# Optimization experiments

Hardware: AMD Instinct MI355X
Metric: run time of the kernel (lower is better)

The kernel has to match this reference:

```python
import jax, jax.numpy as jnp
import numpy as np

C = 128   # channels / dim
NH = 4    # num heads
HD = C // NH
K = 5     # conv kernel size: t=int((log2(128)+1)/2)=4 -> k=5
P = 12    # patch size
GH = 8    # grid height/width (96/12)
NPATCH = GH * GH
FEAT = P * P * C


def _ln(x, g, b):
    m = jnp.mean(x, -1, keepdims=True)
    v = jnp.var(x, -1, keepdims=True)
    return (x - m) / jnp.sqrt(v + 1e-5) * g + b


def _conv1d(x, w, pad):
    return jax.lax.conv_general_dilated(x, w, (1,), [(pad, pad)], dimension_numbers=('NCH', 'OIH', 'NCH'))


def _pool(x, out):
    # exact adaptive avg pool when H % out == 0
    B, c, H, W = x.shape
    f = H // out
    return x.reshape(B, c, out, f, out, f).mean((3, 5))


def _bilinear_ac(x, out):
    # bilinear interpolate [B,C,H,H] -> [B,C,out,out], align_corners=True
    H = x.shape[2]
    cpos = jnp.arange(out) * (H - 1) / (out - 1)
    i0 = jnp.floor(cpos).astype(jnp.int32)
    i1 = jnp.minimum(i0 + 1, H - 1)
    w = (cpos - i0).astype(x.dtype)
    xh = x[:, :, i0, :] * (1 - w)[None, None, :, None] + x[:, :, i1, :] * w[None, None, :, None]
    return xh[:, :, :, i0] * (1 - w) + xh[:, :, :, i1] * w


def setup_inputs() -> dict:
    key = jax.random.key(0)
    ks = jax.random.split(key, 8)
    B = 16
    return {
        's1': jax.random.normal(ks[0], (B, C, 96, 96), jnp.float32),
        'o': jax.random.normal(ks[1], (B, C, 64, 64), jnp.float32),
        'index': jax.random.randint(ks[2], (4, 2), 0, 96),
        'pe_w': jax.random.normal(ks[3], (64, 64, K), jnp.float32) * 0.05,
        'bn_g': jnp.ones((64,), jnp.float32),
        'bn_b': jnp.zeros((64,), jnp.float32),
        'bn_m': jnp.zeros((64,), jnp.float32),
        'bn_v': jnp.ones((64,), jnp.float32),
        'lnx_g': jnp.ones((C,), jnp.float32),
        'lnx_b': jnp.zeros((C,), jnp.float32),
        'lny_g': jnp.ones((C,), jnp.float32),
        'lny_b': jnp.zeros((C,), jnp.float32),
        'qkv_w': jax.random.normal(ks[4], (3 * C, C), jnp.float32) * 0.02,
        'qkv_b': jnp.zeros((3 * C,), jnp.float32),
        'yv_w': jax.random.normal(ks[5], (C, C), jnp.float32) * 0.02,
        'yv_b': jnp.zeros((C,), jnp.float32),
        'proj_w': jax.random.normal(ks[6], (C, C), jnp.float32) * 0.02,
        'proj_b': jnp.zeros((C,), jnp.float32),
        'c1d_w': jax.random.normal(ks[7], (C, C, K), jnp.float32) * 0.05,
    }


def reference(s1, o, index, pe_w, bn_g, bn_b, bn_m, bn_v, lnx_g, lnx_b, lny_g, lny_b,
              qkv_w, qkv_b, yv_w, yv_b, proj_w, proj_b, c1d_w):
    B = s1.shape[0]
    pad = (K - 1) // 2
    # --- mask(s1): patch embedding, conv1d+BN(eval)+ReLU, selective-square mask ---
    # einops: b c (h p1) (w p2) -> b (h w) (p1 p2 c)
    x = s1.reshape(B, C, GH, P, GH, P).transpose(0, 2, 4, 3, 5, 1).reshape(B, NPATCH, FEAT)
    x = _conv1d(x, pe_w, pad)
    x = (x - bn_m[None, :, None]) / jnp.sqrt(bn_v + 1e-5)[None, :, None] * bn_g[None, :, None] + bn_b[None, :, None]
    x = jax.nn.relu(x)
    # mask: rows at center indices keep value (mul by 1), all other rows squared
    idxs = index[:, 0] // P * GH + index[:, 1] // P
    sel = jnp.zeros((NPATCH,), bool).at[idxs].set(True)
    x = x * jnp.where(sel[None, :, None], 1.0, x)
    # einops back: b (h w) (p1 p2 c) -> b c (h p1) (w p2), then pool to 32
    x = x.reshape(B, GH, GH, P, P, C).transpose(0, 5, 1, 3, 2, 4).reshape(B, C, 96, 96)
    short = _pool(x, 32)                                   # [B,C,32,32]
    # --- attention branch ---
    op = _pool(o, 32)
    N = 32 * 32
    of = _ln(op.reshape(B, C, N).transpose(0, 2, 1), lnx_g, lnx_b)   # [B,N,C]
    ori = short.reshape(B, C, N).transpose(0, 2, 1)
    sn = _ln(ori, lny_g, lny_b)
    qkv = (of @ qkv_w.T + qkv_b).reshape(B, N, 3, NH, HD).transpose(2, 0, 3, 1, 4)
    q, k, v = qkv[0], qkv[1], qkv[2]                       # each [B,H,N,D]
    yv = (sn @ yv_w.T + yv_b).reshape(B, N, NH, HD).transpose(0, 2, 1, 3)
    attn = jax.nn.softmax(jnp.einsum('bhnd,bhmd->bhnm', q, k) * HD ** -0.5, axis=-1)
    xv = v + jnp.einsum('bhnm,bhmd->bhnd', attn, yv)
    xv = xv.transpose(0, 2, 1, 3).reshape(B, N, C) @ proj_w.T + proj_b
    xv = (xv + ori).transpose(0, 2, 1)                     # [B,C,N]
    xv = xv + _conv1d(xv, c1d_w, pad)
    xv = xv.reshape(B, C, 32, 32)
    return _bilinear_ac(xv, 96)
```

## Files before the change

kernel.cpp:

```cpp
#include <hip/hip_runtime.h>

#define FEAT 18432

typedef __attribute__((ext_vector_type(8))) short short8;
typedef __attribute__((ext_vector_type(4))) float f32x4;

__device__ __forceinline__ float b2f(unsigned short s) {
  union { unsigned int u; float f; } v; v.u = ((unsigned int)s) << 16; return v.f;
}
__device__ __forceinline__ unsigned short f2bf(float x) {
  union { float f; unsigned int u; } v; v.f = x;
  unsigned int u = v.u;
  unsigned int r = (u + 0x7FFFu + ((u >> 16) & 1u)) >> 16;
  return (unsigned short)r;
}

__device__ __forceinline__ void gl_lds16(const void* g, void* l) {
  __builtin_amdgcn_global_load_lds(
      (const __attribute__((address_space(1))) unsigned int*)g,
      (__attribute__((address_space(3))) unsigned int*)l, 16, 0, 0);
}

__global__ __launch_bounds__(256) void k_transpose(const float* __restrict__ s1,
                                                   unsigned short* __restrict__ xT) {
  int c = blockIdx.x, b = blockIdx.y;
  __shared__ float lds[96 * 99];
  int t = threadIdx.x;
  const float* src = s1 + ((size_t)b * 128 + c) * 9216;
  for (int idx = t; idx < 2304; idx += 256) {
    float4 v = ((const float4*)src)[idx];
    int h = idx / 24, w0 = (idx - h * 24) * 4;
    float* p = lds + h * 99 + w0;
    p[0] = v.x; p[1] = v.y; p[2] = v.z; p[3] = v.w;
  }
  __syncthreads();
  unsigned short* dstb = xT + (size_t)b * FEAT * 64;
  int sw = c & 7;
  for (int idx = t; idx < 1152; idx += 256) {
    int p1p2 = idx >> 3, gh = idx & 7;
    int p1 = p1p2 / 12, p2 = p1p2 - p1 * 12;
    const float* row = lds + (gh * 12 + p1) * 99 + p2;
    uint4 u;
    u.x = f2bf(row[0])  | ((unsigned int)f2bf(row[12]) << 16);
    u.y = f2bf(row[24]) | ((unsigned int)f2bf(row[36]) << 16);
    u.z = f2bf(row[48]) | ((unsigned int)f2bf(row[60]) << 16);
    u.w = f2bf(row[72]) | ((unsigned int)f2bf(row[84]) << 16);
    int f = p1p2 * 128 + c;
    int pos = gh ^ sw;
    *(uint4*)(dstb + (size_t)f * 64 + pos * 8) = u;
  }
}

__global__ __launch_bounds__(256) void k_prep(const float* __restrict__ pe_w,
                                              unsigned short* __restrict__ wpk) {
  int oc0 = blockIdx.x * 8;
  for (int e = threadIdx.x; e < 2560; e += 256) {
    int oc = oc0 + e / 320;
    int kL = e - (e / 320) * 320;
    int ic = kL & 63, kk = kL >> 6;
    float v = pe_w[(oc * 64 + ic) * 5 + kk];
    int LC = kL >> 3;
    int pos = (LC & 56) | ((LC & 7) ^ (oc & 7));
    wpk[oc * 320 + (pos << 3) + (kL & 7)] = f2bf(v);
  }
}

__global__ __launch_bounds__(256) void k_prepc(const float* __restrict__ cw,
                                               float* __restrict__ cwt) {
  int e0 = (blockIdx.x * 256 + threadIdx.x) * 4;
#pragma unroll
  for (int j = 0; j < 4; ++j) {
    int e = e0 + j;
    int r = e >> 7, oc = e & 127;
    cwt[e] = cw[(size_t)oc * 640 + r];
  }
}

__global__ __launch_bounds__(256) void k_prepw(const float* __restrict__ W,
                                               unsigned short* __restrict__ dst,
                                               int ncols) {
  int idx = blockIdx.x * 256 + threadIdx.x;
  if (idx >= ncols * 16) return;
  int n = idx >> 4, c = idx & 15;
  int slot = (c & 8) | ((c & 7) ^ (n & 7));
  const float* s = W + (size_t)n * 128 + c * 8;
  uint4 u;
  u.x = (unsigned int)f2bf(s[0]) | ((unsigned int)f2bf(s[1]) << 16);
  u.y = (unsigned int)f2bf(s[2]) | ((unsigned int)f2bf(s[3]) << 16);
  u.z = (unsigned int)f2bf(s[4]) | ((unsigned int)f2bf(s[5]) << 16);
  u.w = (unsigned int)f2bf(s[6]) | ((unsigned int)f2bf(s[7]) << 16);
  *(uint4*)(dst + (size_t)n * 128 + slot * 8) = u;
}

__global__ __launch_bounds__(256) void k_conv_pe(
    const unsigned short* __restrict__ xT, const unsigned short* __restrict__ wpk,
    const float* __restrict__ bn_g, const float* __restrict__ bn_b,
    const float* __restrict__ bn_m, const float* __restrict__ bn_v,
    const int* __restrict__ indexp, unsigned short* __restrict__ ym) {
  extern __shared__ char smem[];
  unsigned short* Wl = (unsigned short*)smem;
  unsigned short* xl = (unsigned short*)(smem + 40960);
  float* scf = (float*)(smem + 74240);
  float* shf = (float*)(smem + 74496);
  int*   sli = (int*)(smem + 74752);
  int t = threadIdx.x;
  int b = blockIdx.y;
  int blk_f0 = blockIdx.x << 9;
  int lane = t & 63, w = t >> 6;
  int n16 = lane & 15, q = lane >> 4;

  for (int j = 0; j < 10; ++j) {
    int seg = w * 10 + j;
    gl_lds16((const char*)wpk + (seg << 10) + lane * 16, (char*)Wl + (seg << 10));
  }
  if (t < 64) {
    float sc = bn_g[t] * rsqrtf(bn_v[t] + 1e-5f);
    scf[t] = sc;
    shf[t] = bn_b[t] - bn_m[t] * sc;
    int i0 = indexp[0] / 12 * 8 + indexp[1] / 12;
    int i1 = indexp[2] / 12 * 8 + indexp[3] / 12;
    int i2 = indexp[4] / 12 * 8 + indexp[5] / 12;
    int i3 = indexp[6] / 12 * 8 + indexp[7] / 12;
    sli[t] = (t == i0 || t == i1 || t == i2 || t == i3) ? 1 : 0;
  }

  const unsigned short* xb = xT + (size_t)b * FEAT * 64;
  const unsigned int* xbu = (const unsigned int*)xb;

  for (int wnd = 0; wnd < 2; ++wnd) {
    int F0 = blk_f0 + (wnd << 8);
    __syncthreads();
    int flA = (F0 == 0) ? 2 : 0;
    for (int j = 0; j < 8; ++j) {
      int seg = (w << 3) + j;
      int gRow = F0 - 2 + flA + (seg << 3);
      gl_lds16((const char*)xb + (size_t)gRow * 128 + lane * 16,
               (char*)xl + flA * 128 + (seg << 10));
    }
    if (t < 128) {
      int r0 = (flA == 2) ? 0 : 256;
      int fl = (t < 64) ? (r0 + (t >> 5)) : (258 + ((t >> 5) & 1));
      int j = t & 31;
      int f = F0 - 2 + fl;
      unsigned int v = 0;
      if (f >= 0 && f < FEAT) v = xbu[(size_t)f * 32 + j];
      ((unsigned int*)xl)[fl * 32 + j] = v;
    }
    __syncthreads();

    f32x4 acc[4][4];
#pragma unroll
    for (int mt = 0; mt < 4; ++mt)
#pragma unroll
      for (int nt = 0; nt < 4; ++nt) acc[mt][nt] = (f32x4){0.f, 0.f, 0.f, 0.f};

    int rowB = w * 64 + n16;
#pragma unroll
    for (int kk = 0; kk < 5; ++kk) {
      int swb = (n16 + kk + 6) & 7;
#pragma unroll
      for (int ih = 0; ih < 2; ++ih) {
        int ca = (ih << 2) | q;
        const unsigned short* Ap = Wl + kk * 64 + ((ca ^ (n16 & 7)) << 3) + n16 * 320;
        short8 a0 = *(const short8*)(Ap);
        short8 a1 = *(const short8*)(Ap + 16 * 320);
        short8 a2 = *(const short8*)(Ap + 32 * 320);
        short8 a3 = *(const short8*)(Ap + 48 * 320);
        const unsigned short* Bp = xl + ((ca ^ swb) << 3) + (rowB + kk) * 64;
        short8 b0 = *(const short8*)(Bp);
        short8 b1 = *(const short8*)(Bp + 16 * 64);
        short8 b2 = *(const short8*)(Bp + 32 * 64);
        short8 b3 = *(const short8*)(Bp + 48 * 64);
        acc[0][0] = __builtin_amdgcn_mfma_f32_16x16x32_bf16(a0, b0, acc[0][0], 0, 0, 0);
        acc[0][1] = __builtin_amdgcn_mfma_f32_16x16x32_bf16(a0, b1, acc[0][1], 0, 0, 0);
        acc[0][2] = __builtin_amdgcn_mfma_f32_16x16x32_bf16(a0, b2, acc[0][2], 0, 0, 0);
        acc[0][3] = __builtin_amdgcn_mfma_f32_16x16x32_bf16(a0, b3, acc[0][3], 0, 0, 0);
        acc[1][0] = __builtin_amdgcn_mfma_f32_16x16x32_bf16(a1, b0, acc[1][0], 0, 0, 0);
        acc[1][1] = __builtin_amdgcn_mfma_f32_16x16x32_bf16(a1, b1, acc[1][1], 0, 0, 0);
        acc[1][2] = __builtin_amdgcn_mfma_f32_16x16x32_bf16(a1, b2, acc[1][2], 0, 0, 0);
        acc[1][3] = __builtin_amdgcn_mfma_f32_16x16x32_bf16(a1, b3, acc[1][3], 0, 0, 0);
        acc[2][0] = __builtin_amdgcn_mfma_f32_16x16x32_bf16(a2, b0, acc[2][0], 0, 0, 0);
        acc[2][1] = __builtin_amdgcn_mfma_f32_16x16x32_bf16(a2, b1, acc[2][1], 0, 0, 0);
        acc[2][2] = __builtin_amdgcn_mfma_f32_16x16x32_bf16(a2, b2, acc[2][2], 0, 0, 0);
        acc[2][3] = __builtin_amdgcn_mfma_f32_16x16x32_bf16(a2, b3, acc[2][3], 0, 0, 0);
        acc[3][0] = __builtin_amdgcn_mfma_f32_16x16x32_bf16(a3, b0, acc[3][0], 0, 0, 0);
        acc[3][1] = __builtin_amdgcn_mfma_f32_16x16x32_bf16(a3, b1, acc[3][1], 0, 0, 0);
        acc[3][2] = __builtin_amdgcn_mfma_f32_16x16x32_bf16(a3, b2, acc[3][2], 0, 0, 0);
        acc[3][3] = __builtin_amdgcn_mfma_f32_16x16x32_bf16(a3, b3, acc[3][3], 0, 0, 0);
      }
    }

#pragma unroll
    for (int mt = 0; mt < 4; ++mt) {
#pragma unroll
      for (int i = 0; i < 4; ++i) {
        int oc = mt * 16 + q * 4 + i;
        float sc = scf[oc], sh = shf[oc];
        bool sel = sli[oc] != 0;
        unsigned short* yo = ym + ((size_t)b * 64 + oc) * FEAT + F0 + w * 64 + n16;
#pragma unroll
        for (int nt = 0; nt < 4; ++nt) {
          float y = fmaf(acc[mt][nt][i], sc, sh);
          y = fmaxf(y, 0.f);
          if (!sel) y *= y;
          yo[nt * 16] = f2bf(y);
        }
      }
    }
  }
}

__global__ __launch_bounds__(256) void k_pool9ln(
    const unsigned short* __restrict__ ym, const float* __restrict__ lng,
    const float* __restrict__ lnb, float* __restrict__ ori,
    unsigned short* __restrict__ snh) {
  int oc = blockIdx.x, b = blockIdx.y;
  const unsigned short* src = ym + ((size_t)b * 64 + oc) * FEAT;
  int oh0 = (oc >> 3) << 2, ow0 = (oc & 7) << 2;
  __shared__ float red[8];
  int t = threadIdx.x;
  int c = t & 127, hr = t >> 7, wv = t >> 6, l64 = t & 63;
  float g = lng[c], bb = lnb[c];
  for (int p = 0; p < 8; ++p) {
    int nl = p * 2 + hr;
    int pg1 = nl >> 2, pg2 = nl & 3;
    int pbase = (pg1 * 36 + pg2 * 3) * 128 + c;
    float s = 0.f;
#pragma unroll
    for (int dy = 0; dy < 3; ++dy)
#pragma unroll
      for (int dx = 0; dx < 3; ++dx)
        s += b2f(src[pbase + (dy * 12 + dx) * 128]);
    float val = s * (1.f / 9.f);
    float su = val, q = val * val;
#pragma unroll
    for (int off = 32; off > 0; off >>= 1) {
      su += __shfl_xor(su, off, 64);
      q += __shfl_xor(q, off, 64);
    }
    if (l64 == 0) { red[wv * 2] = su; red[wv * 2 + 1] = q; }
    __syncthreads();
    float S = red[hr * 4 + 0] + red[hr * 4 + 2];
    float Q = red[hr * 4 + 1] + red[hr * 4 + 3];
    float mean = S * (1.f / 128.f);
    float var = Q * (1.f / 128.f) - mean * mean;
    float inv = rsqrtf(var + 1e-5f);
    int n = (oh0 + pg1) * 32 + ow0 + pg2;
    size_t base = ((size_t)b * 1024 + n) * 128;
    ori[base + c] = val;
    float lnv = (val - mean) * inv * g + bb;
    int ch = c >> 3;
    int slot = (ch & 8) | ((ch & 7) ^ (n & 7));
    snh[base + slot * 8 + (c & 7)] = f2bf(lnv);
    __syncthreads();
  }
}

__global__ __launch_bounds__(256) void k_poolo_ln(
    const float* __restrict__ o, const float* __restrict__ lng,
    const float* __restrict__ lnb, unsigned short* __restrict__ oflh) {
  int y = blockIdx.x, b = blockIdx.y;
  __shared__ float pl[128 * 33];
  int t = threadIdx.x;
  for (int idx = t; idx < 4096; idx += 256) {
    int xo = idx & 31, c = idx >> 5;
    const float* p = o + (((size_t)b * 128 + c) * 64 + 2 * y) * 64 + 2 * xo;
    float2 a = *(const float2*)p;
    float2 d = *(const float2*)(p + 64);
    pl[c * 33 + xo] = 0.25f * (a.x + a.y + d.x + d.y);
  }
  __syncthreads();
  int xo = t >> 3, l8 = t & 7;
  float v[16]; float s = 0.f, q = 0.f;
#pragma unroll
  for (int i = 0; i < 16; ++i) {
    float x = pl[(l8 * 16 + i) * 33 + xo];
    v[i] = x; s += x; q += x * x;
  }
#pragma unroll
  for (int off = 1; off < 8; off <<= 1) {
    s += __shfl_xor(s, off, 8);
    q += __shfl_xor(q, off, 8);
  }
  float mean = s * (1.f / 128.f);
  float var = q * (1.f / 128.f) - mean * mean;
  float inv = rsqrtf(var + 1e-5f);
  int n = y * 32 + xo;
  unsigned short* dst = oflh + ((size_t)b * 1024 + n) * 128;
  int m7 = n & 7;
#pragma unroll
  for (int h = 0; h < 2; ++h) {
    int c = l8 * 2 + h;
    int slot = (c & 8) | ((c & 7) ^ m7);
    uint4 u;
    float w0 = (v[h * 8 + 0] - mean) * inv * lng[c * 8 + 0] + lnb[c * 8 + 0];
    float w1 = (v[h * 8 + 1] - mean) * inv * lng[c * 8 + 1] + lnb[c * 8 + 1];
    float w2 = (v[h * 8 + 2] - mean) * inv * lng[c * 8 + 2] + lnb[c * 8 + 2];
    float w3 = (v[h * 8 + 3] - mean) * inv * lng[c * 8 + 3] + lnb[c * 8 + 3];
    float w4 = (v[h * 8 + 4] - mean) * inv * lng[c * 8 + 4] + lnb[c * 8 + 4];
    float w5 = (v[h * 8 + 5] - mean) * inv * lng[c * 8 + 5] + lnb[c * 8 + 5];
    float w6 = (v[h * 8 + 6] - mean) * inv * lng[c * 8 + 6] + lnb[c * 8 + 6];
    float w7 = (v[h * 8 + 7] - mean) * inv * lng[c * 8 + 7] + lnb[c * 8 + 7];
    u.x = (unsigned int)f2bf(w0) | ((unsigned int)f2bf(w1) << 16);
    u.y = (unsigned int)f2bf(w2) | ((unsigned int)f2bf(w3) << 16);
    u.z = (unsigned int)f2bf(w4) | ((unsigned int)f2bf(w5) << 16);
    u.w = (unsigned int)f2bf(w6) | ((unsigned int)f2bf(w7) << 16);
    *(uint4*)(dst + slot * 8) = u;
  }
}

__global__ __launch_bounds__(256) void k_gemm_mfma(
    const unsigned short* __restrict__ A, const unsigned short* __restrict__ W,
    const float* __restrict__ bias, float* __restrict__ out, int Ncols) {
  __shared__ unsigned short Al[128 * 128];
  __shared__ unsigned short Bl[64 * 128];
  int m0 = blockIdx.x << 7, n0 = blockIdx.y << 6;
  int t = threadIdx.x;
  int lane = t & 63, w = t >> 6;
  int n16 = lane & 15, q = lane >> 4;

  for (int j = 0; j < 8; ++j) {
    int seg = w * 8 + j;
    gl_lds16((const char*)A + (size_t)m0 * 256 + (seg << 10) + lane * 16,
             (char*)Al + (seg << 10));
  }
  for (int j = 0; j < 4; ++j) {
    int seg = w * 4 + j;
    gl_lds16((const char*)W + (size_t)n0 * 256 + (seg << 10) + lane * 16,
             (char*)Bl + (seg << 10));
  }
  __syncthreads();

  int wm = w >> 1, wn = w & 1;
  f32x4 acc[4][2];
#pragma unroll
  for (int mt = 0; mt < 4; ++mt)
#pragma unroll
    for (int nt = 0; nt < 2; ++nt) acc[mt][nt] = (f32x4){0.f, 0.f, 0.f, 0.f};

#pragma unroll
  for (int kf = 0; kf < 4; ++kf) {
    int ca = kf * 4 + q;
    int rA0 = wm * 64 + n16;
    const unsigned short* Ap0 = Al + (size_t)rA0 * 128;
    int slotA = (ca & 8) | ((ca & 7) ^ (rA0 & 7));
    short8 a0 = *(const short8*)(Ap0 + slotA * 8);
    short8 a1 = *(const short8*)(Ap0 + 16 * 128 + slotA * 8);
    short8 a2 = *(const short8*)(Ap0 + 32 * 128 + slotA * 8);
    short8 a3 = *(const short8*)(Ap0 + 48 * 128 + slotA * 8);
    int rB0 = wn * 32 + n16;
    const unsigned short* Bp0 = Bl + (size_t)rB0 * 128;
    int slotB = (ca & 8) | ((ca & 7) ^ (rB0 & 7));
    short8 b0 = *(const short8*)(Bp0 + slotB * 8);
    short8 b1 = *(const short8*)(Bp0 + 16 * 128 + slotB * 8);
    acc[0][0] = __builtin_amdgcn_mfma_f32_16x16x32_bf16(a0, b0, acc[0][0], 0, 0, 0);
    acc[0][1] = __builtin_amdgcn_mfma_f32_16x16x32_bf16(a0, b1, acc[0][1], 0, 0, 0);
    acc[1][0] = __builtin_amdgcn_mfma_f32_16x16x32_bf16(a1, b0, acc[1][0], 0, 0, 0);
    acc[1][1] = __builtin_amdgcn_mfma_f32_16x16x32_bf16(a1, b1, acc[1][1], 0, 0, 0);
    acc[2][0] = __builtin_amdgcn_mfma_f32_16x16x32_bf16(a2, b0, acc[2][0], 0, 0, 0);
    acc[2][1] = __builtin_amdgcn_mfma_f32_16x16x32_bf16(a2, b1, acc[2][1], 0, 0, 0);
    acc[3][0] = __builtin_amdgcn_mfma_f32_16x16x32_bf16(a3, b0, acc[3][0], 0, 0, 0);
    acc[3][1] = __builtin_amdgcn_mfma_f32_16x16x32_bf16(a3, b1, acc[3][1], 0, 0, 0);
  }

#pragma unroll
  for (int mt = 0; mt < 4; ++mt) {
#pragma unroll
    for (int i = 0; i < 4; ++i) {
      int m = m0 + wm * 64 + mt * 16 + q * 4 + i;
#pragma unroll
      for (int nt = 0; nt < 2; ++nt) {
        int n = n0 + wn * 32 + nt * 16 + n16;
        out[(size_t)m * Ncols + n] = acc[mt][nt][i] + bias[n];
      }
    }
  }
}

__global__ __launch_bounds__(256) void k_cvt(const float* __restrict__ qkv,
                                             const float* __restrict__ yv,
                                             unsigned short* __restrict__ qkb,
                                             unsigned short* __restrict__ vtb) {
  int nt = blockIdx.x, b = blockIdx.y;
  int n0 = nt << 6;
  int t = threadIdx.x;
  __shared__ unsigned short tl[64 * 132];
  const float* qb = qkv + ((size_t)b * 1024 + n0) * 384;
  for (int it = 0; it < 16; ++it) {
    int idx = it * 256 + t;
    int n = idx >> 6, c4 = idx & 63;
    float4 v = *(const float4*)(qb + (size_t)n * 384 + c4 * 4);
    int c = c4 << 2;
    int kind = c >> 7, h = (c >> 5) & 3, d = c & 31;
    uint2 u;
    u.x = (unsigned int)f2bf(v.x) | ((unsigned int)f2bf(v.y) << 16);
    u.y = (unsigned int)f2bf(v.z) | ((unsigned int)f2bf(v.w) << 16);
    *(uint2*)(qkb + ((((size_t)b * 4 + h) * 2 + kind) * 1024 + n0 + n) * 32 + d) = u;
  }
  const float* vb = yv + ((size_t)b * 1024 + n0) * 128;
  for (int it = 0; it < 8; ++it) {
    int idx = it * 256 + t;
    int n = idx >> 5, c4 = idx & 31;
    float4 v = *(const float4*)(vb + (size_t)n * 128 + c4 * 4);
    unsigned short* o = tl + n * 132 + c4 * 4;
    o[0] = f2bf(v.x); o[1] = f2bf(v.y); o[2] = f2bf(v.z); o[3] = f2bf(v.w);
  }
  __syncthreads();
  int c = t >> 1, half = t & 1;
  unsigned short* orow = vtb + (((size_t)b * 4 + (c >> 5)) * 32 + (c & 31)) * 1024 + n0 + half * 32;
#pragma unroll
  for (int k = 0; k < 4; ++k) {
    short8 pack;
#pragma unroll
    for (int j = 0; j < 8; ++j)
      pack[j] = (short)tl[(half * 32 + k * 8 + j) * 132 + c];
    *(short8*)(orow + k * 8) = pack;
  }
}

__global__ __launch_bounds__(256) void k_attn(const float* __restrict__ qkv,
                                              const unsigned short* __restrict__ qkb,
                                              const unsigned short* __restrict__ vtb,
                                              float* __restrict__ att) {
  int qt = blockIdx.x, h = blockIdx.y, b = blockIdx.z;
  __shared__ unsigned short Qs[64 * 40];
  __shared__ unsigned short Ks[64 * 40];
  __shared__ unsigned short Vt[32 * 72];
  __shared__ unsigned short Pw[4 * 16 * 68];
  int t = threadIdx.x;
  int lane = t & 63, w = t >> 6;
  int quad = lane >> 4, l16 = lane & 15;
  const float* qbase = qkv + (size_t)b * 1024 * 384;
  const unsigned short* qrow = qkb + (((size_t)b * 4 + h) * 2 + 0) * 1024 * 32;
  const unsigned short* krow = qkb + (((size_t)b * 4 + h) * 2 + 1) * 1024 * 32;
  const unsigned short* vrow = vtb + ((size_t)b * 4 + h) * 32 * 1024;
  int q0 = qt << 6;
  int hd = h * 32;

  {
    int r = t >> 2, cq = t & 3;
    short8 v = *(const short8*)(qrow + (size_t)(q0 + r) * 32 + cq * 8);
    *(short8*)(Qs + r * 40 + cq * 8) = v;
  }
  __syncthreads();
  short8 aq = *(const short8*)(Qs + (w * 16 + l16) * 40 + quad * 8);

  f32x4 O[2];
  O[0] = (f32x4){0.f, 0.f, 0.f, 0.f};
  O[1] = (f32x4){0.f, 0.f, 0.f, 0.f};
  float mi0 = -1e30f, li0 = 0.f;
  unsigned short* Pme = Pw + w * (16 * 68);
  const float scl = 0.17677669529663688f;

  for (int ci = 0; ci < 16; ++ci) {
    __syncthreads();
    int kn0 = ci << 6;
    {
      int r = t >> 2, cq = t & 3;
      short8 kv = *(const short8*)(krow + (size_t)(kn0 + r) * 32 + cq * 8);
      *(short8*)(Ks + r * 40 + cq * 8) = kv;
      int d = t >> 3, cc = t & 7;
      short8 vv = *(const short8*)(vrow + (size_t)d * 1024 + kn0 + cc * 8);
      *(short8*)(Vt + d * 72 + cc * 8) = vv;
    }
    __syncthreads();

    f32x4 S[4];
#pragma unroll
    for (int nt = 0; nt < 4; ++nt) S[nt] = (f32x4){0.f, 0.f, 0.f, 0.f};
#pragma unroll
    for (int nt = 0; nt < 4; ++nt) {
      short8 bk = *(const short8*)(Ks + (nt * 16 + l16) * 40 + quad * 8);
      S[nt] = __builtin_amdgcn_mfma_f32_16x16x32_bf16(bk, aq, S[nt], 0, 0, 0);
    }

    float sv[16];
#pragma unroll
    for (int nt = 0; nt < 4; ++nt)
#pragma unroll
      for (int r = 0; r < 4; ++r) sv[nt * 4 + r] = S[nt][r] * scl;
    float m0 = fmaxf(fmaxf(sv[0], sv[1]), fmaxf(sv[2], sv[3]));
    float m1 = fmaxf(fmaxf(sv[4], sv[5]), fmaxf(sv[6], sv[7]));
    float m2 = fmaxf(fmaxf(sv[8], sv[9]), fmaxf(sv[10], sv[11]));
    float m3 = fmaxf(fmaxf(sv[12], sv[13]), fmaxf(sv[14], sv[15]));
    float rm = fmaxf(fmaxf(m0, m1), fmaxf(m2, m3));
    rm = fmaxf(rm, __shfl_xor(rm, 16));
    rm = fmaxf(rm, __shfl_xor(rm, 32));
    float nm = fmaxf(mi0, rm);
    float alpha = __expf(mi0 - nm);
    mi0 = nm;

    float psnt[4];
    unsigned short* pwr = Pme + l16 * 68 + quad * 4;
#pragma unroll
    for (int nt = 0; nt < 4; ++nt) {
      float p0 = __expf(sv[nt * 4 + 0] - nm);
      float p1 = __expf(sv[nt * 4 + 1] - nm);
      float p2 = __expf(sv[nt * 4 + 2] - nm);
      float p3 = __expf(sv[nt * 4 + 3] - nm);
      psnt[nt] = (p0 + p1) + (p2 + p3);
      uint2 u;
      u.x = (unsigned int)f2bf(p0) | ((unsigned int)f2bf(p1) << 16);
      u.y = (unsigned int)f2bf(p2) | ((unsigned int)f2bf(p3) << 16);
      *(uint2*)(pwr + nt * 16) = u;
    }
    float ps = (psnt[0] + psnt[1]) + (psnt[2] + psnt[3]);
    ps += __shfl_xor(ps, 16);
    ps += __shfl_xor(ps, 32);
    li0 = li0 * alpha + ps;

    float al0 = __shfl(alpha, quad * 4 + 0);
    float al1 = __shfl(alpha, quad * 4 + 1);
    float al2 = __shfl(alpha, quad * 4 + 2);
    float al3 = __shfl(alpha, quad * 4 + 3);
    O[0][0] *= al0; O[1][0] *= al0;
    O[0][1] *= al1; O[1][1] *= al1;
    O[0][2] *= al2; O[1][2] *= al2;
    O[0][3] *= al3; O[1][3] *= al3;

#pragma unroll
    for (int kc = 0; kc < 2; ++kc) {
      short8 bv0 = *(const short8*)(Vt + l16 * 72 + kc * 32 + quad * 8);
      short8 bv1 = *(const short8*)(Vt + (16 + l16) * 72 + kc * 32 + quad * 8);
      short8 ap = *(const short8*)(Pme + l16 * 68 + kc * 32 + quad * 8);
      O[0] = __builtin_amdgcn_mfma_f32_16x16x32_bf16(ap, bv0, O[0], 0, 0, 0);
      O[1] = __builtin_amdgcn_mfma_f32_16x16x32_bf16(ap, bv1, O[1], 0, 0, 0);
    }
  }

#pragma unroll
  for (int reg = 0; reg < 4; ++reg) {
    float lit = __shfl(li0, quad * 4 + reg);
    int n = q0 + w * 16 + quad * 4 + reg;
    float inv = 1.f / lit;
#pragma unroll
    for (int nt = 0; nt < 2; ++nt) {
      int dd = hd + nt * 16 + l16;
      float val = O[nt][reg] * inv + qbase[(size_t)n * 384 + 256 + dd];
      att[((size_t)b * 1024 + n) * 128 + dd] = val;
    }
  }
}

__global__ __launch_bounds__(256) void k_proj(
    const float* __restrict__ att, const float* __restrict__ proj_w,
    const float* __restrict__ proj_b, const float* __restrict__ ori,
    float* __restrict__ xv2) {
  int nt = blockIdx.x, b = blockIdx.y;
  int n0 = nt << 6;
  __shared__ float Al[64 * 67], Wl[128 * 67];
  int t = threadIdx.x, tn = t & 15, tc = t >> 4;
  float acc[4][8];
#pragma unroll
  for (int i = 0; i < 4; ++i)
#pragma unroll
    for (int j = 0; j < 8; ++j) acc[i][j] = 0.f;
  const float* Ab = att + ((size_t)b * 1024 + n0) * 128;
  for (int kc = 0; kc < 2; ++kc) {
    __syncthreads();
    for (int idx = t; idx < 4096; idx += 256) {
      int r = idx >> 6, kk = idx & 63;
      Al[r * 67 + kk] = Ab[(size_t)r * 128 + kc * 64 + kk];
    }
    for (int idx = t; idx < 8192; idx += 256) {
      int r = idx >> 6, kk = idx & 63;
      Wl[r * 67 + kk] = proj_w[(size_t)r * 128 + kc * 64 + kk];
    }
    __syncthreads();
    for (int kk = 0; kk < 64; ++kk) {
      float a[4], w[8];
#pragma unroll
      for (int i = 0; i < 4; ++i) a[i] = Al[(tn * 4 + i) * 67 + kk];
#pragma unroll
      for (int j = 0; j < 8; ++j) w[j] = Wl[(tc * 8 + j) * 67 + kk];
#pragma unroll
      for (int i = 0; i < 4; ++i)
#pragma unroll
        for (int j = 0; j < 8; ++j) acc[i][j] = fmaf(a[i], w[j], acc[i][j]);
    }
  }
#pragma unroll
  for (int j = 0; j < 8; ++j) {
    int c = tc * 8 + j;
    float pb = proj_b[c];
    float4 vv;
    vv.x = acc[0][j] + pb + ori[((size_t)b * 1024 + n0 + tn * 4 + 0) * 128 + c];
    vv.y = acc[1][j] + pb + ori[((size_t)b * 1024 + n0 + tn * 4 + 1) * 128 + c];
    vv.z = acc[2][j] + pb + ori[((size_t)b * 1024 + n0 + tn * 4 + 2) * 128 + c];
    vv.w = acc[3][j] + pb + ori[((size_t)b * 1024 + n0 + tn * 4 + 3) * 128 + c];
    *(float4*)(xv2 + ((size_t)b * 128 + c) * 1024 + n0 + tn * 4) = vv;
  }
}

__global__ __launch_bounds__(256) void k_conv1d(
    const float* __restrict__ xv2, const float* __restrict__ cwt,
    float* __restrict__ xv3) {
  extern __shared__ char cs[];
  float* xl = (float*)cs;
  float* wl = (float*)(cs + 18432);
  int nt = blockIdx.x, b = blockIdx.y;
  int n0 = nt << 5;
  int t = threadIdx.x;
  int lane = t & 63, w = t >> 6;
  const float* xb = xv2 + (size_t)b * 128 * 1024;
  for (int idx = t; idx < 4608; idx += 256) {
    int ic = idx / 36, j = idx - ic * 36;
    int n = n0 + j - 2;
    xl[idx] = (n >= 0 && n < 1024) ? xb[(size_t)ic * 1024 + n] : 0.f;
  }

  int oc = t & 127, g = t >> 7;
  float acc[16];
#pragma unroll
  for (int i = 0; i < 16; ++i) acc[i] = 0.f;

#pragma unroll 1
  for (int ch = 0; ch < 16; ++ch) {
    __syncthreads();
#pragma unroll
    for (int j = 0; j < 5; ++j) {
      int seg = w * 5 + j;
      gl_lds16((const char*)cwt + (size_t)ch * 20480 + (seg << 10) + lane * 16,
               (char*)wl + (seg << 10));
    }
    __syncthreads();

#pragma unroll
    for (int icl = 0; icl < 8; ++icl) {
      int ic = ch * 8 + icl;
      const float* xr = xl + ic * 36 + (g << 4);
      float xw[20];
#pragma unroll
      for (int q2 = 0; q2 < 5; ++q2) {
        float4 v = *(const float4*)(xr + q2 * 4);
        xw[q2 * 4] = v.x; xw[q2 * 4 + 1] = v.y; xw[q2 * 4 + 2] = v.z; xw[q2 * 4 + 3] = v.w;
      }
      const float* wr = wl + icl * 5 * 128 + oc;
      float w0 = wr[0], w1 = wr[128], w2 = wr[256], w3 = wr[384], w4 = wr[512];
#pragma unroll
      for (int i = 0; i < 16; ++i)
        acc[i] = fmaf(xw[i], w0, fmaf(xw[i + 1], w1, fmaf(xw[i + 2], w2,
                 fmaf(xw[i + 3], w3, fmaf(xw[i + 4], w4, acc[i])))));
    }
  }

  const float* res = xb + (size_t)oc * 1024 + n0 + (g << 4);
  float* outp = xv3 + ((size_t)b * 128 + oc) * 1024 + n0 + (g << 4);
#pragma unroll
  for (int q2 = 0; q2 < 4; ++q2) {
    float4 r = *(const float4*)(res + q2 * 4);
    float4 o_;
    o_.x = r.x + acc[q2 * 4 + 0];
    o_.y = r.y + acc[q2 * 4 + 1];
    o_.z = r.z + acc[q2 * 4 + 2];
    o_.w = r.w + acc[q2 * 4 + 3];
    *(float4*)(outp + q2 * 4) = o_;
  }
}

__global__ __launch_bounds__(256) void k_bilinear(const float* __restrict__ xv3,
                                                  float* __restrict__ out) {
  int idx = blockIdx.x * 256 + threadIdx.x;
  int X = idx % 96;
  int t2 = idx / 96;
  int Y = t2 % 96;
  int bc = t2 / 96;
  const float* src = xv3 + (size_t)bc * 1024;
  const float r = 31.f / 95.f;
  float py = Y * r, px = X * r;
  int y0 = (int)py, x0 = (int)px;
  float wy = py - y0, wx = px - x0;
  int y1 = y0 < 31 ? y0 + 1 : 31, x1 = x0 < 31 ? x0 + 1 : 31;
  float a = src[y0 * 32 + x0], b_ = src[y0 * 32 + x1];
  float c_ = src[y1 * 32 + x0], d_ = src[y1 * 32 + x1];
  float t0 = a * (1.f - wy) + c_ * wy;
  float t1 = b_ * (1.f - wy) + d_ * wy;
  out[idx] = t0 * (1.f - wx) + t1 * wx;
}

extern "C" void kernel_launch(void* const* d_in, const int* in_sizes, int n_in,
                              void* d_out, int out_size, void* d_ws, size_t ws_size,
                              hipStream_t stream) {
  (void)in_sizes; (void)n_in; (void)out_size; (void)ws_size;
  const float* s1    = (const float*)d_in[0];
  const float* o     = (const float*)d_in[1];
  const int*   indx  = (const int*)d_in[2];
  const float* pe_w  = (const float*)d_in[3];
  const float* bn_g  = (const float*)d_in[4];
  const float* bn_b  = (const float*)d_in[5];
  const float* bn_m  = (const float*)d_in[6];
  const float* bn_v  = (const float*)d_in[7];
  const float* lnx_g = (const float*)d_in[8];
  const float* lnx_b = (const float*)d_in[9];
  const float* lny_g = (const float*)d_in[10];
  const float* lny_b = (const float*)d_in[11];
  const float* qkv_w = (const float*)d_in[12];
  const float* qkv_b = (const float*)d_in[13];
  const float* yv_w  = (const float*)d_in[14];
  const float* yv_b  = (const float*)d_in[15];
  const float* proj_w = (const float*)d_in[16];
  const float* proj_b = (const float*)d_in[17];
  const float* c1d_w  = (const float*)d_in[18];

  char* ws = (char*)d_ws;
  unsigned short* xTh = (unsigned short*)ws;
  unsigned short* ymh = (unsigned short*)(ws + 37748736);
  unsigned short* wpk = (unsigned short*)d_out;
  float* cwt = (float*)((char*)d_out + 65536);
  unsigned short* wqkh = (unsigned short*)((char*)d_out + 458752);
  unsigned short* wyvh = (unsigned short*)((char*)d_out + 573440);
  float* ori  = (float*)ws;
  unsigned short* snh  = (unsigned short*)(ws + 8388608);
  unsigned short* oflh = (unsigned short*)(ws + 16777216);
  float* attb = (float*)(ws + 25165824);
  float* qkvb  = (float*)(ws + 37748736);
  float* yvbuf = (float*)(ws + 62914560);
  unsigned short* qkb = (unsigned short*)(ws + 16777216);
  unsigned short* vtb = (unsigned short*)(ws + 71303168);
  float* xv2   = (float*)(ws + 37748736);
  float* xv3   = (float*)(ws + 46137344);

  hipLaunchKernelGGL(k_prep, dim3(8), dim3(256), 0, stream, pe_w, wpk);
  hipLaunchKernelGGL(k_prepc, dim3(80), dim3(256), 0, stream, c1d_w, cwt);
  hipLaunchKernelGGL(k_prepw, dim3(24), dim3(256), 0, stream, qkv_w, wqkh, 384);
  hipLaunchKernelGGL(k_prepw, dim3(8), dim3(256), 0, stream, yv_w, wyvh, 128);
  hipLaunchKernelGGL(k_transpose, dim3(128, 16), dim3(256), 0, stream, s1, xTh);
  hipLaunchKernelGGL(k_conv_pe, dim3(36, 16), dim3(256), 75008, stream,
                     xTh, wpk, bn_g, bn_b, bn_m, bn_v, indx, ymh);
  hipLaunchKernelGGL(k_pool9ln, dim3(64, 16), dim3(256), 0, stream, ymh, lny_g, lny_b, ori, snh);
  hipLaunchKernelGGL(k_poolo_ln, dim3(32, 16), dim3(256), 0, stream, o, lnx_g, lnx_b, oflh);
  hipLaunchKernelGGL(k_gemm_mfma, dim3(128, 6), dim3(256), 0, stream, oflh, wqkh, qkv_b, qkvb, 384);
  hipLaunchKernelGGL(k_gemm_mfma, dim3(128, 2), dim3(256), 0, stream, snh, wyvh, yv_b, yvbuf, 128);
  hipLaunchKernelGGL(k_cvt, dim3(16, 16), dim3(256), 0, stream, qkvb, yvbuf, qkb, vtb);
  hipLaunchKernelGGL(k_attn, dim3(16, 4, 16), dim3(256), 0, stream, qkvb, qkb, vtb, attb);
  hipLaunchKernelGGL(k_proj, dim3(16, 16), dim3(256), 0, stream, attb, proj_w, proj_b, ori, xv2);
  hipLaunchKernelGGL(k_conv1d, dim3(32, 16), dim3(256), 38912, stream, xv2, cwt, xv3);
  hipLaunchKernelGGL(k_bilinear, dim3(73728), dim3(256), 0, stream, xv3, (float*)d_out);
}
```

Before: 411.9 us.

## Replace scalar FP32 projection GEMM with bf16 MFMA kernel fed by swizzled attention output

The attention kernel now writes its output as bf16 in a swizzled row layout instead of fp32. A new MFMA-based projection kernel loads that output and a bf16-packed proj_w directly into LDS and computes the projection with matrix-core instructions. The bias and residual add and the transposed write are kept. This replaces the scalar-FMA fp32 GEMM and halves the intermediate traffic, at the cost of bf16 rounding on the attention output and one extra weight-prep launch.

```diff
diff --git a/kernel.cpp b/kernel.cpp
--- a/kernel.cpp
+++ b/kernel.cpp
@@ -377,6 +377,81 @@
   }
 }
 
+__global__ __launch_bounds__(256) void k_proj_mfma(
+    const unsigned short* __restrict__ A, const unsigned short* __restrict__ W,
+    const float* __restrict__ bias, const float* __restrict__ ori,
+    float* __restrict__ xv2) {
+  __shared__ unsigned short Al[128 * 128];
+  __shared__ unsigned short Bl[64 * 128];
+  int m0 = blockIdx.x << 7, n0 = blockIdx.y << 6;
+  int t = threadIdx.x;
+  int lane = t & 63, w = t >> 6;
+  int n16 = lane & 15, q = lane >> 4;
+
+  for (int j = 0; j < 8; ++j) {
+    int seg = w * 8 + j;
+    gl_lds16((const char*)A + (size_t)m0 * 256 + (seg << 10) + lane * 16,
+             (char*)Al + (seg << 10));
+  }
+  for (int j = 0; j < 4; ++j) {
+    int seg = w * 4 + j;
+    gl_lds16((const char*)W + (size_t)n0 * 256 + (seg << 10) + lane * 16,
+             (char*)Bl + (seg << 10));
+  }
+  __syncthreads();
+
+  int wm = w >> 1, wn = w & 1;
+  f32x4 acc[4][2];
+#pragma unroll
+  for (int mt = 0; mt < 4; ++mt)
+#pragma unroll
+    for (int nt = 0; nt < 2; ++nt) acc[mt][nt] = (f32x4){0.f, 0.f, 0.f, 0.f};
+
+#pragma unroll
+  for (int kf = 0; kf < 4; ++kf) {
+    int ca = kf * 4 + q;
+    int rA0 = wm * 64 + n16;
+    const unsigned short* Ap0 = Al + (size_t)rA0 * 128;
+    int slotA = (ca & 8) | ((ca & 7) ^ (rA0 & 7));
+    short8 a0 = *(const short8*)(Ap0 + slotA * 8);
+    short8 a1 = *(const short8*)(Ap0 + 16 * 128 + slotA * 8);
+    short8 a2 = *(const short8*)(Ap0 + 32 * 128 + slotA * 8);
+    short8 a3 = *(const short8*)(Ap0 + 48 * 128 + slotA * 8);
+    int rB0 = wn * 32 + n16;
+    const unsigned short* Bp0 = Bl + (size_t)rB0 * 128;
+    int slotB = (ca & 8) | ((ca & 7) ^ (rB0 & 7));
+    short8 b0 = *(const short8*)(Bp0 + slotB * 8);
+    short8 b1 = *(const short8*)(Bp0 + 16 * 128 + slotB * 8);
+    acc[0][0] = __builtin_amdgcn_mfma_f32_16x16x32_bf16(a0, b0, acc[0][0], 0, 0, 0);
+    acc[0][1] = __builtin_amdgcn_mfma_f32_16x16x32_bf16(a0, b1, acc[0][1], 0, 0, 0);
+    acc[1][0] = __builtin_amdgcn_mfma_f32_16x16x32_bf16(a1, b0, acc[1][0], 0, 0, 0);
+    acc[1][1] = __builtin_amdgcn_mfma_f32_16x16x32_bf16(a1, b1, acc[1][1], 0, 0, 0);
+    acc[2][0] = __builtin_amdgcn_mfma_f32_16x16x32_bf16(a2, b0, acc[2][0], 0, 0, 0);
+    acc[2][1] = __builtin_amdgcn_mfma_f32_16x16x32_bf16(a2, b1, acc[2][1], 0, 0, 0);
+    acc[3][0] = __builtin_amdgcn_mfma_f32_16x16x32_bf16(a3, b0, acc[3][0], 0, 0, 0);
+    acc[3][1] = __builtin_amdgcn_mfma_f32_16x16x32_bf16(a3, b1, acc[3][1], 0, 0, 0);
+  }
+
+  int bb = m0 >> 10;
+  int nbase = (m0 & 1023) + wm * 64;
+#pragma unroll
+  for (int mt = 0; mt < 4; ++mt) {
+    int nloc = nbase + mt * 16 + q * 4;
+    const float* orow = ori + ((size_t)bb * 1024 + nloc) * 128;
+#pragma unroll
+    for (int nt = 0; nt < 2; ++nt) {
+      int c = n0 + wn * 32 + nt * 16 + n16;
+      float pb = bias[c];
+      float4 vv;
+      vv.x = acc[mt][nt][0] + pb + orow[c];
+      vv.y = acc[mt][nt][1] + pb + orow[128 + c];
+      vv.z = acc[mt][nt][2] + pb + orow[256 + c];
+      vv.w = acc[mt][nt][3] + pb + orow[384 + c];
+      *(float4*)(xv2 + ((size_t)bb * 128 + c) * 1024 + nloc) = vv;
+    }
+  }
+}
+
 __global__ __launch_bounds__(256) void k_cvt(const float* __restrict__ qkv,
                                              const float* __restrict__ yv,
                                              unsigned short* __restrict__ qkb,
@@ -421,7 +496,7 @@
 __global__ __launch_bounds__(256) void k_attn(const float* __restrict__ qkv,
                                               const unsigned short* __restrict__ qkb,
                                               const unsigned short* __restrict__ vtb,
-                                              float* __restrict__ att) {
+                                              unsigned short* __restrict__ atth) {
   int qt = blockIdx.x, h = blockIdx.y, b = blockIdx.z;
   __shared__ unsigned short Qs[64 * 40];
   __shared__ unsigned short Ks[64 * 40];
@@ -533,62 +608,16 @@
     float lit = __shfl(li0, quad * 4 + reg);
     int n = q0 + w * 16 + quad * 4 + reg;
     float inv = 1.f / lit;
+    size_t mrow = ((size_t)b * 1024 + n) * 128;
+    int m7 = n & 7;
 #pragma unroll
     for (int nt = 0; nt < 2; ++nt) {
       int dd = hd + nt * 16 + l16;
       float val = O[nt][reg] * inv + qbase[(size_t)n * 384 + 256 + dd];
-      att[((size_t)b * 1024 + n) * 128 + dd] = val;
-    }
-  }
-}
-
-__global__ __launch_bounds__(256) void k_proj(
-    const float* __restrict__ att, const float* __restrict__ proj_w,
-    const float* __restrict__ proj_b, const float* __restrict__ ori,
-    float* __restrict__ xv2) {
-  int nt = blockIdx.x, b = blockIdx.y;
-  int n0 = nt << 6;
-  __shared__ float Al[64 * 67], Wl[128 * 67];
-  int t = threadIdx.x, tn = t & 15, tc = t >> 4;
-  float acc[4][8];
-#pragma unroll
-  for (int i = 0; i < 4; ++i)
-#pragma unroll
-    for (int j = 0; j < 8; ++j) acc[i][j] = 0.f;
-  const float* Ab = att + ((size_t)b * 1024 + n0) * 128;
-  for (int kc = 0; kc < 2; ++kc) {
-    __syncthreads();
-    for (int idx = t; idx < 4096; idx += 256) {
-      int r = idx >> 6, kk = idx & 63;
-      Al[r * 67 + kk] = Ab[(size_t)r * 128 + kc * 64 + kk];
-    }
-    for (int idx = t; idx < 8192; idx += 256) {
-      int r = idx >> 6, kk = idx & 63;
-      Wl[r * 67 + kk] = proj_w[(size_t)r * 128 + kc * 64 + kk];
-    }
-    __syncthreads();
-    for (int kk = 0; kk < 64; ++kk) {
-      float a[4], w[8];
-#pragma unroll
-      for (int i = 0; i < 4; ++i) a[i] = Al[(tn * 4 + i) * 67 + kk];
-#pragma unroll
-      for (int j = 0; j < 8; ++j) w[j] = Wl[(tc * 8 + j) * 67 + kk];
-#pragma unroll
-      for (int i = 0; i < 4; ++i)
-#pragma unroll
-        for (int j = 0; j < 8; ++j) acc[i][j] = fmaf(a[i], w[j], acc[i][j]);
-    }
-  }
-#pragma unroll
-  for (int j = 0; j < 8; ++j) {
-    int c = tc * 8 + j;
-    float pb = proj_b[c];
-    float4 vv;
-    vv.x = acc[0][j] + pb + ori[((size_t)b * 1024 + n0 + tn * 4 + 0) * 128 + c];
-    vv.y = acc[1][j] + pb + ori[((size_t)b * 1024 + n0 + tn * 4 + 1) * 128 + c];
-    vv.z = acc[2][j] + pb + ori[((size_t)b * 1024 + n0 + tn * 4 + 2) * 128 + c];
-    vv.w = acc[3][j] + pb + ori[((size_t)b * 1024 + n0 + tn * 4 + 3) * 128 + c];
-    *(float4*)(xv2 + ((size_t)b * 128 + c) * 1024 + n0 + tn * 4) = vv;
+      int ch = dd >> 3;
+      int slot = (ch & 8) | ((ch & 7) ^ m7);
+      atth[mrow + slot * 8 + (dd & 7)] = f2bf(val);
+    }
   }
 }
 
@@ -709,10 +738,11 @@
   float* cwt = (float*)((char*)d_out + 65536);
   unsigned short* wqkh = (unsigned short*)((char*)d_out + 458752);
   unsigned short* wyvh = (unsigned short*)((char*)d_out + 573440);
+  unsigned short* wprh = (unsigned short*)((char*)d_out + 622592);
   float* ori  = (float*)ws;
   unsigned short* snh  = (unsigned short*)(ws + 8388608);
   unsigned short* oflh = (unsigned short*)(ws + 16777216);
-  float* attb = (float*)(ws + 25165824);
+  unsigned short* atth = (unsigned short*)(ws + 25165824);
   float* qkvb  = (float*)(ws + 37748736);
   float* yvbuf = (float*)(ws + 62914560);
   unsigned short* qkb = (unsigned short*)(ws + 16777216);
@@ -724,6 +754,7 @@
   hipLaunchKernelGGL(k_prepc, dim3(80), dim3(256), 0, stream, c1d_w, cwt);
   hipLaunchKernelGGL(k_prepw, dim3(24), dim3(256), 0, stream, qkv_w, wqkh, 384);
   hipLaunchKernelGGL(k_prepw, dim3(8), dim3(256), 0, stream, yv_w, wyvh, 128);
+  hipLaunchKernelGGL(k_prepw, dim3(8), dim3(256), 0, stream, proj_w, wprh, 128);
   hipLaunchKernelGGL(k_transpose, dim3(128, 16), dim3(256), 0, stream, s1, xTh);
   hipLaunchKernelGGL(k_conv_pe, dim3(36, 16), dim3(256), 75008, stream,
                      xTh, wpk, bn_g, bn_b, bn_m, bn_v, indx, ymh);
@@ -732,8 +763,8 @@
   hipLaunchKernelGGL(k_gemm_mfma, dim3(128, 6), dim3(256), 0, stream, oflh, wqkh, qkv_b, qkvb, 384);
   hipLaunchKernelGGL(k_gemm_mfma, dim3(128, 2), dim3(256), 0, stream, snh, wyvh, yv_b, yvbuf, 128);
   hipLaunchKernelGGL(k_cvt, dim3(16, 16), dim3(256), 0, stream, qkvb, yvbuf, qkb, vtb);
-  hipLaunchKernelGGL(k_attn, dim3(16, 4, 16), dim3(256), 0, stream, qkvb, qkb, vtb, attb);
-  hipLaunchKernelGGL(k_proj, dim3(16, 16), dim3(256), 0, stream, attb, proj_w, proj_b, ori, xv2);
+  hipLaunchKernelGGL(k_attn, dim3(16, 4, 16), dim3(256), 0, stream, qkvb, qkb, vtb, atth);
+  hipLaunchKernelGGL(k_proj_mfma, dim3(128, 2), dim3(256), 0, stream, atth, wprh, proj_b, ori, xv2);
   hipLaunchKernelGGL(k_conv1d, dim3(32, 16), dim3(256), 38912, stream, xv2, cwt, xv3);
   hipLaunchKernelGGL(k_bilinear, dim3(73728), dim3(256), 0, stream, xv3, (float*)d_out);
 }
```

Measured after the change: 393.6 us. 4.4% less time.
